# Optimization experiments

Measured on AMD Instinct MI355X. Metric: run time of the kernel, lower is better.

Reference implementation:

```python
import jax, jax.numpy as jnp
import numpy as np

HID, DSTATE, K, DIN, HDIM, NH, CHUNK = 2048, 128, 4, 4096, 64, 64, 256
CONVD = DIN + 2 * DSTATE  # 4352
EPS = 1e-5


def setup_inputs() -> dict:
    key = jax.random.key(0)
    ks = jax.random.split(key, 10)
    B, L = 2, 4096
    hidden_states = jax.random.normal(ks[0], (B, L, HID), jnp.float32)
    proj_out = 2 * (DIN + DSTATE) + NH  # 8512
    in_proj_w = jax.random.normal(ks[1], (proj_out, HID), jnp.float32) * (HID ** -0.5)
    conv_w = jax.random.normal(ks[2], (CONVD, K), jnp.float32) * (K ** -0.5)
    conv_b = jax.random.normal(ks[3], (CONVD,), jnp.float32) * 0.01
    dt_bias = jax.random.uniform(ks[4], (NH,), jnp.float32)
    A = jax.random.uniform(ks[5], (NH,), jnp.float32, minval=1.0, maxval=16.0)
    A_log = jnp.log(A)
    D = jnp.ones((NH,), jnp.float32)
    norm_w = jnp.ones((DIN,), jnp.float32)
    out_proj_w = jax.random.normal(ks[6], (HID, DIN), jnp.float32) * (DIN ** -0.5)
    return {"hidden_states": hidden_states, "in_proj_w": in_proj_w, "conv_w": conv_w,
            "conv_b": conv_b, "dt_bias": dt_bias, "A_log": A_log, "D": D,
            "norm_w": norm_w, "out_proj_w": out_proj_w}


def _segsum(x):
    # x: [..., L] -> [..., L, L] lower-triangular cumulative sums, -inf above diag
    Lc = x.shape[-1]
    cs = jnp.cumsum(x, -1)
    seg = cs[..., :, None] - cs[..., None, :]
    mask = jnp.tril(jnp.ones((Lc, Lc), bool))
    return jnp.where(mask, seg, -jnp.inf)


def _causal_conv1d(x, w, b):
    # x: [B, L, D] depthwise causal conv, kernel K, then SiLU
    L = x.shape[1]
    xp = jnp.pad(x, ((0, 0), (K - 1, 0), (0, 0)))
    y = sum(xp[:, i:i + L, :] * w[:, i] for i in range(K)) + b
    return jax.nn.silu(y)


def _ssd(x, Bm, Cm, dt, A, D):
    # x:[b,l,h,p]  Bm,Cm:[b,l,n]  dt:[b,l,h] (post-softplus)  A:[h]  D:[h]
    b, l, h, p = x.shape
    n = Bm.shape[-1]
    c = l // CHUNK
    xr = x.reshape(b, c, CHUNK, h, p)
    Br = Bm.reshape(b, c, CHUNK, n)
    Cr = Cm.reshape(b, c, CHUNK, n)
    dtr = dt.reshape(b, c, CHUNK, h)
    Adt = jnp.transpose(dtr * A, (0, 3, 1, 2))          # [b,h,c,L]
    Acs = jnp.cumsum(Adt, -1)                            # [b,h,c,L]
    Lmat = jnp.exp(_segsum(Adt))                         # [b,h,c,L,L]
    xdt = xr * dtr[..., None]                            # [b,c,L,h,p]
    # intra-chunk (diagonal) term
    Yd = jnp.einsum('bcln,bcsn,bhcls,bcshp->bclhp', Cr, Br, Lmat, xdt)
    # per-chunk final states
    decay_states = jnp.exp(Acs[..., -1:] - Acs)          # [b,h,c,L]
    chunk_states = jnp.einsum('bcln,bhcl,bclhp->bchpn', Br, decay_states, xdt)
    chunk_decay = jnp.exp(Acs[..., -1])                  # [b,h,c]
    def step(state, inp):
        dec, cs = inp
        return state * dec[..., None, None] + cs, state
    init = jnp.zeros((b, h, p, n), x.dtype)
    _, prev = jax.lax.scan(step, init,
                           (jnp.moveaxis(chunk_decay, -1, 0), jnp.moveaxis(chunk_states, 1, 0)))
    prev = jnp.moveaxis(prev, 0, 1)                      # [b,c,h,p,n] state entering each chunk
    Yo = jnp.einsum('bcln,bchpn,bhcl->bclhp', Cr, prev, jnp.exp(Acs))
    Y = Yd + Yo + xr * D[:, None]
    return Y.reshape(b, l, h * p)


def _gated_rmsnorm(y, z, w):
    y32 = y.astype(jnp.float32) * jax.nn.silu(z.astype(jnp.float32))
    var = jnp.mean(y32 * y32, -1, keepdims=True)
    return (y32 * jax.lax.rsqrt(var + EPS) * w).astype(y.dtype)


def reference(hidden_states, in_proj_w, conv_w, conv_b, dt_bias, A_log, D, norm_w, out_proj_w):
    zxbcdt = hidden_states @ in_proj_w.T                 # [b,l,8512]
    z = zxbcdt[..., :DIN]
    xBC = zxbcdt[..., DIN:DIN + CONVD]
    dt = zxbcdt[..., DIN + CONVD:]                       # [b,l,h]
    xBC = _causal_conv1d(xBC, conv_w, conv_b)
    x = xBC[..., :DIN]
    Bm = xBC[..., DIN:DIN + DSTATE]
    Cm = xBC[..., DIN + DSTATE:]
    A = -jnp.exp(A_log)
    dt = jax.nn.softplus(dt + dt_bias)
    b, l, _ = x.shape
    y = _ssd(x.reshape(b, l, NH, HDIM), Bm, Cm, dt, A, D)
    y = _gated_rmsnorm(y, z, norm_w)
    return y @ out_proj_w.T
```

## Files before the change

kernel.cpp:

```cpp
#include <hip/hip_runtime.h>
#include <hip/hip_bf16.h>


typedef __bf16 v8bf __attribute__((ext_vector_type(8)));
typedef float  v4f  __attribute__((ext_vector_type(4)));

#define LL long long

__device__ inline v8bf load8(const float* p) {
    v4f a = *(const v4f*)p, b = *(const v4f*)(p + 4);
    v8bf r;
#pragma unroll
    for (int i = 0; i < 4; ++i) { r[i] = (__bf16)a[i]; r[i + 4] = (__bf16)b[i]; }
    return r;
}

__device__ __forceinline__ void gload_lds16(const __bf16* g, __bf16* l) {
    __builtin_amdgcn_global_load_lds(
        (const __attribute__((address_space(1))) void*)g,
        (__attribute__((address_space(3))) void*)l, 16, 0, 0);
}

__global__ __launch_bounds__(256) void cast_bf16_kernel(
    const float* __restrict__ in, __bf16* __restrict__ out)
{
    LL i = ((LL)blockIdx.x * 256 + threadIdx.x) * 8;
    *(v8bf*)&out[i] = load8(&in[i]);
}

__global__ __launch_bounds__(256) void cast_split_kernel(
    const float* __restrict__ in, __bf16* __restrict__ hi,
    __bf16* __restrict__ lo)
{
    LL i = ((LL)blockIdx.x * 256 + threadIdx.x) * 8;
    v4f a = *(const v4f*)&in[i], b = *(const v4f*)&in[i + 4];
    v8bf h, l;
#pragma unroll
    for (int k = 0; k < 4; ++k) {
        __bf16 hh = (__bf16)a[k];  h[k]     = hh;  l[k]     = (__bf16)(a[k] - (float)hh);
        __bf16 hb = (__bf16)b[k];  h[k + 4] = hb;  l[k + 4] = (__bf16)(b[k] - (float)hb);
    }
    *(v8bf*)&hi[i] = h;
    *(v8bf*)&lo[i] = l;
}

template <int MODE, int TM, int TN, int RN>
__global__ __launch_bounds__(512, 2) void gemm_bt_8p(
    const __bf16* __restrict__ Ab, const __bf16* __restrict__ Bb, int KT,
    int lda, int ldb,
    __bf16* __restrict__ z_out, __bf16* __restrict__ x_out,
    float* __restrict__ outf, int ldc)
{
    __shared__ __align__(16) __bf16 lds[65536];
    constexpr int RM = 8 / RN;
    constexpr int LM = TM / RM, LN = TN / RN;
    const int orig = blockIdx.x;
    const int x = orig & 7, loc = orig >> 3;
    const int M0 = ((x / RN) * LM + loc / LN) * 256;
    const int N0 = ((x % RN) * LN + loc % LN) * 256;

    const int tid  = threadIdx.x;
    const int lane = tid & 63, wave = tid >> 6;
    const int wr = wave >> 2, wc = wave & 3;
    const int lrow = lane & 15, quad = lane >> 4;
    const int row0 = tid >> 3;
    const int g0   = (tid & 7) ^ (row0 & 7);

    v4f acc[8][4] = {};
    v8bf aF[2][4], b0F[2][2], b1F[2][2];

#define STAGE_A(par, half, kt) do { \
    const __bf16* _s = Ab + (size_t)(M0 + (half)*128 + row0) * lda + (kt)*64 + g0*8; \
    __bf16* _d = lds + ((par)*2 + (half)) * 8192 + wave * 512; \
    gload_lds16(_s, _d); \
    gload_lds16(_s + (size_t)64 * lda, _d + 4096); \
} while (0)

#define STAGE_B(par, half, kt) do { \
    const __bf16* _s = Bb + (size_t)(N0 + (half)*128 + row0) * ldb + (kt)*64 + g0*8; \
    __bf16* _d = lds + 32768 + ((par)*2 + (half)) * 8192 + wave * 512; \
    gload_lds16(_s, _d); \
    gload_lds16(_s + (size_t)64 * ldb, _d + 4096); \
} while (0)

#define READ_A(par, qm) do { \
    const __bf16* _s = lds + ((par)*2 + wr) * 8192; \
    _Pragma("unroll") \
    for (int _ks = 0; _ks < 2; ++_ks) \
      _Pragma("unroll") \
      for (int _m = 0; _m < 4; ++_m) \
        aF[_ks][_m] = *(const v8bf*)&_s[((qm)*64 + _m*16 + lrow)*64 + \
                                        ((((_ks<<2)+quad) ^ (lrow&7))<<3)]; \
} while (0)

#define READ_B(par, qn, DST) do { \
    const __bf16* _s = lds + 32768 + ((par)*2 + (wc>>1)) * 8192; \
    _Pragma("unroll") \
    for (int _ks = 0; _ks < 2; ++_ks) \
      _Pragma("unroll") \
      for (int _n = 0; _n < 2; ++_n) \
        DST[_ks][_n] = *(const v8bf*)&_s[((wc&1)*64 + (qn)*32 + _n*16 + lrow)*64 + \
                                         ((((_ks<<2)+quad) ^ (lrow&7))<<3)]; \
} while (0)

#define MFQ(qm, qn, BF) do { \
    __builtin_amdgcn_s_setprio(1); \
    _Pragma("unroll") \
    for (int _ks = 0; _ks < 2; ++_ks) \
      _Pragma("unroll") \
      for (int _m = 0; _m < 4; ++_m) \
        _Pragma("unroll") \
        for (int _n = 0; _n < 2; ++_n) \
          acc[(qm)*4+_m][(qn)*2+_n] = __builtin_amdgcn_mfma_f32_16x16x32_bf16( \
              aF[_ks][_m], BF[_ks][_n], acc[(qm)*4+_m][(qn)*2+_n], 0, 0, 0); \
    __builtin_amdgcn_s_setprio(0); \
} while (0)

#define PBAR  __builtin_amdgcn_s_barrier()
#define LGKM0 asm volatile("s_waitcnt lgkmcnt(0)" ::: "memory")
#define VMC4  asm volatile("s_waitcnt vmcnt(4)" ::: "memory")
#define VMC0  asm volatile("s_waitcnt vmcnt(0)" ::: "memory")

    STAGE_A(0, 0, 0); STAGE_A(0, 1, 0); STAGE_B(0, 0, 0); STAGE_B(0, 1, 0);
    STAGE_A(1, 0, 1); STAGE_B(1, 0, 1);
    VMC4; PBAR;

    const int KT2 = KT >> 1;
    for (int it = 0; it < KT2; ++it) {
        const int T0 = 2 * it, T1 = 2 * it + 1;
        const bool notlast = (it < KT2 - 1);
        READ_A(0, 0); READ_B(0, 0, b0F);
        STAGE_A(1, 1, T1);
        PBAR; LGKM0; MFQ(0, 0, b0F); PBAR;
        READ_B(0, 1, b1F);
        STAGE_B(1, 1, T1);
        PBAR; LGKM0; MFQ(0, 1, b1F); PBAR;
        READ_A(0, 1);
        if (notlast) STAGE_B(0, 0, T0 + 2);
        PBAR; LGKM0; MFQ(1, 0, b0F); PBAR;
        if (notlast) STAGE_A(0, 0, T0 + 2);
        PBAR; LGKM0; MFQ(1, 1, b1F);
        if (notlast) { VMC4; } else { VMC0; }
        PBAR;
        READ_A(1, 0); READ_B(1, 0, b0F);
        if (notlast) STAGE_A(0, 1, T0 + 2);
        PBAR; LGKM0; MFQ(0, 0, b0F); PBAR;
        READ_B(1, 1, b1F);
        if (notlast) STAGE_B(0, 1, T0 + 2);
        PBAR; LGKM0; MFQ(0, 1, b1F); PBAR;
        READ_A(1, 1);
        if (notlast) STAGE_B(1, 0, T1 + 2);
        PBAR; LGKM0; MFQ(1, 0, b0F); PBAR;
        if (notlast) STAGE_A(1, 0, T1 + 2);
        PBAR; LGKM0; MFQ(1, 1, b1F);
        if (notlast) { VMC4; } else { VMC0; }
        PBAR;
    }

#undef STAGE_A
#undef STAGE_B
#undef READ_A
#undef READ_B
#undef MFQ

#pragma unroll
    for (int m = 0; m < 8; ++m)
#pragma unroll
        for (int n = 0; n < 4; ++n)
#pragma unroll
            for (int r = 0; r < 4; ++r) {
                int row = M0 + wr * 128 + m * 16 + quad * 4 + r;
                int col = N0 + wc * 64 + n * 16 + lrow;
                float v = acc[m][n][r];
                if constexpr (MODE == 1) {
                    if (col < 4096) z_out[(LL)row * 4096 + col] = (__bf16)v;
                    else            x_out[(LL)row * 4096 + (col - 4096)] = (__bf16)v;
                } else {
                    outf[(LL)row * ldc + col] = v;
                }
            }
}

__global__ __launch_bounds__(256) void bcdt_gemm_kernel(
    const __bf16* __restrict__ Ahi, const __bf16* __restrict__ Alo,
    const __bf16* __restrict__ Whi, const __bf16* __restrict__ Wlo,
    const float* __restrict__ dtbi,
    float* __restrict__ bcr, float* __restrict__ dt)
{
    __shared__ __align__(16) __bf16 sAh[128 * 64];
    __shared__ __align__(16) __bf16 sAl[128 * 64];
    __shared__ __align__(16) __bf16 sWh[64 * 64];
    __shared__ __align__(16) __bf16 sWl[64 * 64];
    const int orig = blockIdx.x;
    const int swz = (orig & 7) * 40 + (orig >> 3);
    const int m0 = (swz / 5) * 128;
    const int n0 = (swz % 5) * 64;
    const int tid = threadIdx.x;
    const int lane = tid & 63, wave = tid >> 6;
    const int lrow = lane & 15, quad = lane >> 4;
    const int wm = wave * 32;
    v4f acc[2][4] = {};

    for (int k0 = 0; k0 < 2048; k0 += 64) {
#pragma unroll
        for (int i = 0; i < 4; ++i) {
            int e = tid + i * 256;
            int row = e >> 3, g = (e & 7) ^ (row & 7);
            const LL so = (LL)(m0 + row) * 2048 + k0 + g * 8;
            gload_lds16(&Ahi[so], &sAh[wave * 512 + i * 2048]);
            gload_lds16(&Alo[so], &sAl[wave * 512 + i * 2048]);
        }
#pragma unroll
        for (int i = 0; i < 2; ++i) {
            int e = tid + i * 256;
            int row = e >> 3, g = (e & 7) ^ (row & 7);
            const LL so = (LL)(n0 + row) * 2048 + k0 + g * 8;
            gload_lds16(&Whi[so], &sWh[wave * 512 + i * 2048]);
            gload_lds16(&Wlo[so], &sWl[wave * 512 + i * 2048]);
        }
        __syncthreads();
#pragma unroll
        for (int ks = 0; ks < 2; ++ks) {
            v8bf ah[2], al[2], wh[4], wl[4];
#pragma unroll
            for (int i = 0; i < 2; ++i) {
                int r = wm + i * 16 + lrow;
                int c = ((((ks << 2) + quad) ^ (lrow & 7)) << 3);
                ah[i] = *(const v8bf*)&sAh[r * 64 + c];
                al[i] = *(const v8bf*)&sAl[r * 64 + c];
            }
#pragma unroll
            for (int j = 0; j < 4; ++j) {
                int r = j * 16 + lrow;
                int c = ((((ks << 2) + quad) ^ (lrow & 7)) << 3);
                wh[j] = *(const v8bf*)&sWh[r * 64 + c];
                wl[j] = *(const v8bf*)&sWl[r * 64 + c];
            }
#pragma unroll
            for (int i = 0; i < 2; ++i)
#pragma unroll
                for (int j = 0; j < 4; ++j) {
                    acc[i][j] = __builtin_amdgcn_mfma_f32_16x16x32_bf16(ah[i], wh[j], acc[i][j], 0, 0, 0);
                    acc[i][j] = __builtin_amdgcn_mfma_f32_16x16x32_bf16(ah[i], wl[j], acc[i][j], 0, 0, 0);
                    acc[i][j] = __builtin_amdgcn_mfma_f32_16x16x32_bf16(al[i], wh[j], acc[i][j], 0, 0, 0);
                }
        }
        __syncthreads();
    }
#pragma unroll
    for (int i = 0; i < 2; ++i)
#pragma unroll
        for (int j = 0; j < 4; ++j)
#pragma unroll
            for (int r = 0; r < 4; ++r) {
                int row = m0 + wm + i * 16 + quad * 4 + r;
                int sc = n0 + j * 16 + lrow;
                float v = acc[i][j][r];
                if (sc < 256) {
                    bcr[(LL)row * 256 + sc] = v;
                } else {
                    float x = v + dtbi[sc - 256];
                    dt[row * 64 + (sc - 256)] = (x > 20.f) ? x : log1pf(__expf(x));
                }
            }
}

__global__ __launch_bounds__(256) void conv_x_kernel(
    const __bf16* __restrict__ xp, const float* __restrict__ cw,
    const float* __restrict__ cbias, __bf16* __restrict__ xq)
{
    int ch = blockIdx.x * 256 + threadIdx.x;
    int l = blockIdx.y, b = blockIdx.z;
    float acc = cbias[ch];
#pragma unroll
    for (int i = 0; i < 4; ++i) {
        int ls = l - 3 + i;
        if (ls >= 0)
            acc += (float)xp[((LL)b * 4096 + ls) * 4096 + ch] * cw[ch * 4 + i];
    }
    acc = acc / (1.f + __expf(-acc));
    xq[((LL)b * 4096 + l) * 4096 + ch] = (__bf16)acc;
}

__global__ __launch_bounds__(256) void conv_bc_kernel(
    const float* __restrict__ bcr, const float* __restrict__ cw,
    const float* __restrict__ cbias, float* __restrict__ bcc)
{
    int ch = threadIdx.x;
    int l = blockIdx.y, b = blockIdx.z;
    float acc = cbias[4096 + ch];
#pragma unroll
    for (int i = 0; i < 4; ++i) {
        int ls = l - 3 + i;
        if (ls >= 0)
            acc += bcr[((LL)b * 4096 + ls) * 256 + ch] * cw[(4096 + ch) * 4 + i];
    }
    acc = acc / (1.f + __expf(-acc));
    bcc[((LL)b * 4096 + l) * 256 + ch] = acc;
}

__global__ __launch_bounds__(256) void cumsum_kernel(
    const float* __restrict__ dt, const float* __restrict__ alog,
    float* __restrict__ acs, float* __restrict__ cdec)
{
    int h = blockIdx.x, c = blockIdx.y, b = blockIdx.z;
    int s = threadIdx.x;
    __shared__ float buf[256];
    float Av = -expf(alog[h]);
    int bl = b * 4096 + c * 256 + s;
    buf[s] = dt[bl * 64 + h] * Av;
    __syncthreads();
    for (int off = 1; off < 256; off <<= 1) {
        float v = (s >= off) ? buf[s - off] : 0.f;
        __syncthreads();
        buf[s] += v;
        __syncthreads();
    }
    int abase = (((b * 16) + c) * 64 + h) * 256;
    acs[abase + s] = buf[s];
    if (s == 255) cdec[(b * 64 + h) * 16 + c] = expf(buf[s]);
}

__global__ __launch_bounds__(256) void chunk_state_kernel(
    const __bf16* __restrict__ xq, const float* __restrict__ bcc,
    const float* __restrict__ dtb, const float* __restrict__ acs,
    float* __restrict__ cs)
{
    int h = blockIdx.x, c = blockIdx.y, b = blockIdx.z;
    int t = threadIdx.x;
    int lg = t & 63, pg = t >> 6;
    int n0 = lg * 2;
    __shared__ __align__(16) float xdt_s[64 * 68];
    __shared__ float dec_s[64];
    const LL lbase = (LL)b * 4096 + c * 256;
    const int abase = (((b * 16) + c) * 64 + h) * 256;
    float alast = acs[abase + 255];
    float a0[16] = {}, a1[16] = {};
    for (int st = 0; st < 4; ++st) {
        for (int i = 0; i < 16; ++i) {
            int e = t + i * 256; int sp = e >> 6, p = e & 63;
            LL row = lbase + st * 64 + sp;
            xdt_s[sp * 68 + p] = (float)xq[row * 4096 + h * 64 + p] * dtb[(row << 6) + h];
        }
        if (t < 64) dec_s[t] = __expf(alast - acs[abase + st * 64 + t]);
        __syncthreads();
        for (int sp = 0; sp < 64; ++sp) {
            LL row = lbase + st * 64 + sp;
            float2 bb = *(const float2*)&bcc[row * 256 + n0];
            float dd = dec_s[sp];
            float b0 = bb.x * dd, b1 = bb.y * dd;
#pragma unroll
            for (int q = 0; q < 4; ++q) {
                v4f xv = *(const v4f*)&xdt_s[sp * 68 + pg * 16 + q * 4];
#pragma unroll
                for (int j = 0; j < 4; ++j) { a0[q * 4 + j] += b0 * xv[j]; a1[q * 4 + j] += b1 * xv[j]; }
            }
        }
        __syncthreads();
    }
    const LL obase = ((LL)(((b * 16) + c) * 64 + h)) * 8192;
    for (int pp = 0; pp < 16; ++pp) {
        int p = pg * 16 + pp;
        cs[obase + p * 128 + n0]     = a0[pp];
        cs[obase + p * 128 + n0 + 1] = a1[pp];
    }
}

__global__ __launch_bounds__(256) void scan_kernel(
    float* __restrict__ cs, const float* __restrict__ cdec)
{
    int h = blockIdx.x, b = blockIdx.y;
    int t = threadIdx.x;
    float st[32];
#pragma unroll
    for (int i = 0; i < 32; ++i) st[i] = 0.f;
    for (int c = 0; c < 16; ++c) {
        LL base = ((LL)(((b * 16) + c) * 64 + h)) * 8192;
        float cd = cdec[(b * 64 + h) * 16 + c];
#pragma unroll
        for (int i = 0; i < 32; ++i) {
            int e = i * 256 + t;
            float v = cs[base + e];
            cs[base + e] = st[i];
            st[i] = st[i] * cd + v;
        }
    }
}

__global__ __launch_bounds__(256) void cb_kernel(const float* __restrict__ bcc,
                                                 float* __restrict__ cbt)
{
    int bx = blockIdx.x;
    int st = bx & 3, lh = bx >> 2;
    int c = blockIdx.y, b = blockIdx.z;
    int t = threadIdx.x;
    int lg = t & 63, pg = t >> 6;
    __shared__ float cr_s[128 * 33];
    __shared__ __align__(16) float brT[32 * 68];
    const LL lbase = (LL)b * 4096 + c * 256;
    const int l0 = lh * 128;
    float acc[2][16] = {};
    for (int nt = 0; nt < 4; ++nt) {
        for (int i = 0; i < 16; ++i) {
            int e = t + i * 256; int l = e >> 5, np = e & 31;
            cr_s[l * 33 + np] = bcc[(lbase + l0 + l) * 256 + 128 + nt * 32 + np];
        }
        for (int i = 0; i < 8; ++i) {
            int e = t + i * 256; int sp = e >> 5, np = e & 31;
            brT[np * 68 + sp] = bcc[(lbase + st * 64 + sp) * 256 + nt * 32 + np];
        }
        __syncthreads();
        for (int np = 0; np < 32; ++np) {
            float w0 = cr_s[lg * 33 + np], w1 = cr_s[(lg + 64) * 33 + np];
#pragma unroll
            for (int q = 0; q < 4; ++q) {
                v4f bv = *(const v4f*)&brT[np * 68 + pg * 16 + q * 4];
#pragma unroll
                for (int j = 0; j < 4; ++j) {
                    acc[0][q * 4 + j] += w0 * bv[j];
                    acc[1][q * 4 + j] += w1 * bv[j];
                }
            }
        }
        __syncthreads();
    }
    const LL obase = ((LL)((b * 16) + c)) * 65536;
#pragma unroll
    for (int r = 0; r < 2; ++r)
        for (int sp = 0; sp < 16; ++sp) {
            int s = st * 64 + pg * 16 + sp;
            cbt[obase + (LL)s * 256 + (l0 + lg + r * 64)] = acc[r][sp];
        }
}

__global__ __launch_bounds__(256) void ssd_y_kernel(
    __bf16* __restrict__ xq, const float* __restrict__ bcc,
    const float* __restrict__ dtb, const float* __restrict__ acs,
    const float* __restrict__ cbt, const float* __restrict__ prevS,
    const float* __restrict__ Dv)
{
    const int h = blockIdx.x, c = blockIdx.y, b = blockIdx.z;
    const int t = threadIdx.x;
    const int lane = t & 63, wave = t >> 6;
    const int lrow = lane & 15, quad = lane >> 4;
    const int wm = wave * 64;
    __shared__ __align__(16) __bf16 As[256][72];
    __shared__ __align__(16) __bf16 Bs[64 * 64];
    __shared__ float acs_s[256];
    __shared__ float qbuf[4][64];
    const LL lbase = (LL)b * 4096 + c * 256;
    const int abase = (((b * 16) + c) * 64 + h) * 256;
    acs_s[t] = acs[abase + t];
    __syncthreads();
    qbuf[t >> 6][t & 63] = __expf(acs_s[(t >> 6) * 64 + 63] - acs_s[t]);
    const float acl_t = acs_s[t];
    const float ea_t  = __expf(acl_t);
    __syncthreads();
    const LL cbbase = ((LL)((b * 16) + c)) * 65536;
    const LL pbase  = ((LL)(((b * 16) + c) * 64 + h)) * 8192;
    v4f acc[4][4] = {};

    for (int kb = 0; kb < 6; ++kb) {
        if (kb < 4) {
            const int sb = kb * 64;
            if (kb < wave) {
                const float r = __expf(acl_t - acs_s[sb + 63]);
#pragma unroll
                for (int g = 0; g < 8; ++g) {
                    v8bf wv;
#pragma unroll
                    for (int u = 0; u < 8; ++u) {
                        float cbv = cbt[cbbase + (LL)(sb + g * 8 + u) * 256 + t];
                        wv[u] = (__bf16)(cbv * (r * qbuf[kb][g * 8 + u]));
                    }
                    *(v8bf*)&As[t][g * 8] = wv;
                }
            } else if (kb == wave) {
#pragma unroll
                for (int g = 0; g < 8; ++g) {
                    v8bf wv;
#pragma unroll
                    for (int u = 0; u < 8; ++u) {
                        int s = sb + g * 8 + u;
                        float cbv = cbt[cbbase + (LL)s * 256 + t];
                        float d = acl_t - acs_s[s];
                        wv[u] = (__bf16)((s <= t) ? cbv * __expf(d) : 0.f);
                    }
                    *(v8bf*)&As[t][g * 8] = wv;
                }
            }
#pragma unroll
            for (int i = 0; i < 16; ++i) {
                int e = t + i * 256; int p = e & 63, sp = e >> 6;
                LL row = lbase + sb + sp;
                float xv = (float)xq[row * 4096 + h * 64 + p] * dtb[((int)row) * 64 + h];
                Bs[p * 64 + ((((sp >> 3) ^ (p & 7)) << 3) | (sp & 7))] = (__bf16)xv;
            }
        } else {
            const int nb = (kb - 4) * 64;
            const LL cb0 = (lbase + t) * 256 + 128 + nb;
#pragma unroll
            for (int g = 0; g < 8; ++g) {
                v4f c0 = *(const v4f*)&bcc[cb0 + g * 8];
                v4f c1 = *(const v4f*)&bcc[cb0 + g * 8 + 4];
                v8bf wv;
#pragma unroll
                for (int u = 0; u < 4; ++u) {
                    wv[u]     = (__bf16)(c0[u] * ea_t);
                    wv[u + 4] = (__bf16)(c1[u] * ea_t);
                }
                *(v8bf*)&As[t][g * 8] = wv;
            }
#pragma unroll
            for (int i = 0; i < 16; ++i) {
                int e = t + i * 256; int n = e & 63, p = e >> 6;
                float pv = prevS[pbase + (LL)p * 128 + nb + n];
                Bs[p * 64 + ((((n >> 3) ^ (p & 7)) << 3) | (n & 7))] = (__bf16)pv;
            }
        }
        __syncthreads();
        if (kb >= 4 || wave >= kb) {
#pragma unroll
            for (int ks = 0; ks < 2; ++ks) {
                v8bf af[4], bfv[4];
#pragma unroll
                for (int i = 0; i < 4; ++i)
                    af[i] = *(const v8bf*)&As[wm + i * 16 + lrow][ks * 32 + quad * 8];
#pragma unroll
                for (int j = 0; j < 4; ++j) {
                    int p = j * 16 + lrow;
                    int kg = (ks * 4 + quad) ^ (p & 7);
                    bfv[j] = *(const v8bf*)&Bs[p * 64 + kg * 8];
                }
#pragma unroll
                for (int i = 0; i < 4; ++i)
#pragma unroll
                    for (int j = 0; j < 4; ++j)
                        acc[i][j] = __builtin_amdgcn_mfma_f32_16x16x32_bf16(af[i], bfv[j], acc[i][j], 0, 0, 0);
            }
        }
        __syncthreads();
    }
    const float Dh = Dv[h];
#pragma unroll
    for (int i = 0; i < 4; ++i)
#pragma unroll
        for (int j = 0; j < 4; ++j)
#pragma unroll
            for (int r = 0; r < 4; ++r) {
                int l = wm + i * 16 + quad * 4 + r;
                int p = j * 16 + lrow;
                LL idx = (lbase + l) * 4096 + h * 64 + p;
                float v = acc[i][j][r] + Dh * (float)xq[idx];
                xq[idx] = (__bf16)v;
            }
}

__global__ __launch_bounds__(256) void rmsnorm_kernel(
    __bf16* __restrict__ y, const __bf16* __restrict__ z,
    const float* __restrict__ nw)
{
    LL r = blockIdx.x;
    int t = threadIdx.x;
    float vals[16]; float ss = 0.f;
#pragma unroll
    for (int i = 0; i < 16; ++i) {
        int j = i * 256 + t;
        float yv = (float)y[r * 4096 + j];
        float zv = (float)z[r * 4096 + j];
        float v = yv * (zv / (1.f + __expf(-zv)));
        vals[i] = v; ss += v * v;
    }
#pragma unroll
    for (int off = 32; off >= 1; off >>= 1) ss += __shfl_down(ss, off, 64);
    __shared__ float red[4];
    if ((t & 63) == 0) red[t >> 6] = ss;
    __syncthreads();
    float tot = red[0] + red[1] + red[2] + red[3];
    float rstd = rsqrtf(tot * (1.f / 4096.f) + 1e-5f);
#pragma unroll
    for (int i = 0; i < 16; ++i) {
        int j = i * 256 + t;
        y[r * 4096 + j] = (__bf16)(vals[i] * rstd * nw[j]);
    }
}

extern "C" void kernel_launch(void* const* d_in, const int* in_sizes, int n_in,
                              void* d_out, int out_size, void* d_ws, size_t ws_size,
                              hipStream_t stream) {
    const float* hs    = (const float*)d_in[0];
    const float* w1    = (const float*)d_in[1];
    const float* cw    = (const float*)d_in[2];
    const float* cbias = (const float*)d_in[3];
    const float* dtbi  = (const float*)d_in[4];
    const float* alog  = (const float*)d_in[5];
    const float* Dv    = (const float*)d_in[6];
    const float* nw    = (const float*)d_in[7];
    const float* wo    = (const float*)d_in[8];
    float* out = (float*)d_out;
    (void)in_sizes; (void)n_in; (void)out_size; (void)ws_size;

    char* ws = (char*)d_ws;
    size_t off = 0;
    auto alloc = [&](size_t bytes) { void* p = ws + off; off += (bytes + 255) & ~(size_t)255; return p; };
    __bf16* xp_b  = (__bf16*)alloc((size_t)8192 * 4096 * 2);
    __bf16* xq_b  = (__bf16*)alloc((size_t)8192 * 4096 * 2);
    float*  bcr_f = (float*) alloc((size_t)8192 * 256 * 4);
    float*  bcc_f = (float*) alloc((size_t)8192 * 256 * 4);
    float*  dt_f  = (float*) alloc((size_t)8192 * 64 * 4);
    float*  acs_f = (float*) alloc((size_t)2 * 16 * 64 * 256 * 4);
    float*  cd_f  = (float*) alloc((size_t)2 * 64 * 16 * 4);
    float*  cbt_f = (float*) alloc((size_t)2 * 16 * 256 * 256 * 4);
    float*  cs_f  = (float*)xp_b;
    __bf16* z_b   = (__bf16*)d_out;

    __bf16* hs_b  = xq_b;
    __bf16* w1_b  = xq_b + (size_t)8192 * 2048;
    __bf16* hs_lo = (__bf16*)xp_b;
    __bf16* ws_hi = hs_lo + (size_t)8192 * 2048;
    __bf16* ws_lo = ws_hi + (size_t)320 * 2048;
    __bf16* wo_b  = (__bf16*)xp_b;

    cast_split_kernel<<<8192, 256, 0, stream>>>(hs, hs_b, hs_lo);
    cast_bf16_kernel<<<8192, 256, 0, stream>>>(w1, w1_b);
    cast_split_kernel<<<320, 256, 0, stream>>>(w1 + (size_t)8192 * 2048, ws_hi, ws_lo);
    bcdt_gemm_kernel<<<320, 256, 0, stream>>>(hs_b, hs_lo, ws_hi, ws_lo,
                                              dtbi, bcr_f, dt_f);
    gemm_bt_8p<1, 32, 32, 4><<<dim3(1024), 512, 0, stream>>>(
        hs_b, w1_b, 32, 2048, 2048, z_b, xp_b, nullptr, 0);
    conv_x_kernel<<<dim3(16, 4096, 2), 256, 0, stream>>>(xp_b, cw, cbias, xq_b);
    conv_bc_kernel<<<dim3(1, 4096, 2), 256, 0, stream>>>(bcr_f, cw, cbias, bcc_f);
    cumsum_kernel<<<dim3(64, 16, 2), 256, 0, stream>>>(dt_f, alog, acs_f, cd_f);
    chunk_state_kernel<<<dim3(64, 16, 2), 256, 0, stream>>>(xq_b, bcc_f, dt_f, acs_f, cs_f);
    scan_kernel<<<dim3(64, 2), 256, 0, stream>>>(cs_f, cd_f);
    cb_kernel<<<dim3(8, 16, 2), 256, 0, stream>>>(bcc_f, cbt_f);
    ssd_y_kernel<<<dim3(64, 16, 2), 256, 0, stream>>>(xq_b, bcc_f, dt_f, acs_f, cbt_f, cs_f, Dv);
    cast_bf16_kernel<<<4096, 256, 0, stream>>>(wo, wo_b);
    rmsnorm_kernel<<<8192, 256, 0, stream>>>(xq_b, z_b, nw);
    gemm_bt_8p<2, 32, 8, 1><<<dim3(256), 512, 0, stream>>>(
        xq_b, wo_b, 64, 4096, 4096, nullptr, nullptr, out, 2048);
}
```

Before: 1.458 ms.

## Split SSD output kernel by row halves and skip upper-triangular CB tiles

The CB kernel now stores its output row-major (l-major) with vectorized float4 writes and launches only the 6 lower-triangular tiles. The SSD output kernel is split into two 128-thread blocks per chunk, each handling half the rows, so it skips the causally masked key blocks. It reads CB rows with vector loads and XOR-swizzles the A tile in shared memory. This removes wasted triangular work and strided global reads, in exchange for twice as many blocks and redundant loads of the B tile across the halves.

Measured after the change: 1.180 ms. 19.0% less time.

```diff
diff --git a/kernel.cpp b/kernel.cpp
--- a/kernel.cpp
+++ b/kernel.cpp
@@ -391,7 +391,8 @@
                                                  float* __restrict__ cbt)
 {
     int bx = blockIdx.x;
-    int st = bx & 3, lh = bx >> 2;
+    int lh = (bx < 2) ? 0 : 1;
+    int st = (bx < 2) ? bx : bx - 2;
     int c = blockIdx.y, b = blockIdx.z;
     int t = threadIdx.x;
     int lg = t & 63, pg = t >> 6;
@@ -399,7 +400,7 @@
     __shared__ __align__(16) float brT[32 * 68];
     const LL lbase = (LL)b * 4096 + c * 256;
     const int l0 = lh * 128;
-    float acc[2][16] = {};
+    v4f acc[2][4] = {};
     for (int nt = 0; nt < 4; ++nt) {
         for (int i = 0; i < 16; ++i) {
             int e = t + i * 256; int l = e >> 5, np = e & 31;
@@ -415,90 +416,106 @@
 #pragma unroll
             for (int q = 0; q < 4; ++q) {
                 v4f bv = *(const v4f*)&brT[np * 68 + pg * 16 + q * 4];
-#pragma unroll
-                for (int j = 0; j < 4; ++j) {
-                    acc[0][q * 4 + j] += w0 * bv[j];
-                    acc[1][q * 4 + j] += w1 * bv[j];
-                }
+                acc[0][q] += w0 * bv;
+                acc[1][q] += w1 * bv;
             }
         }
         __syncthreads();
     }
     const LL obase = ((LL)((b * 16) + c)) * 65536;
 #pragma unroll
-    for (int r = 0; r < 2; ++r)
-        for (int sp = 0; sp < 16; ++sp) {
-            int s = st * 64 + pg * 16 + sp;
-            cbt[obase + (LL)s * 256 + (l0 + lg + r * 64)] = acc[r][sp];
-        }
-}
-
-__global__ __launch_bounds__(256) void ssd_y_kernel(
+    for (int r = 0; r < 2; ++r) {
+        LL rowb = obase + (LL)(l0 + lg + r * 64) * 256 + st * 64 + pg * 16;
+#pragma unroll
+        for (int q = 0; q < 4; ++q)
+            *(v4f*)&cbt[rowb + q * 4] = acc[r][q];
+    }
+}
+
+__global__ __launch_bounds__(128) void ssd_y_kernel(
     __bf16* __restrict__ xq, const float* __restrict__ bcc,
     const float* __restrict__ dtb, const float* __restrict__ acs,
-    const float* __restrict__ cbt, const float* __restrict__ prevS,
+    const float* __restrict__ cbtT, const float* __restrict__ prevS,
     const float* __restrict__ Dv)
 {
-    const int h = blockIdx.x, c = blockIdx.y, b = blockIdx.z;
+    const int h = blockIdx.x;
+    const int c = blockIdx.y >> 1, lh = blockIdx.y & 1;
+    const int b = blockIdx.z;
     const int t = threadIdx.x;
     const int lane = t & 63, wave = t >> 6;
     const int lrow = lane & 15, quad = lane >> 4;
-    const int wm = wave * 64;
-    __shared__ __align__(16) __bf16 As[256][72];
+    const int rb = lh * 2 + wave;
+    const int l = lh * 128 + t;
+    __shared__ __align__(16) __bf16 As[128 * 64];
     __shared__ __align__(16) __bf16 Bs[64 * 64];
     __shared__ float acs_s[256];
     __shared__ float qbuf[4][64];
     const LL lbase = (LL)b * 4096 + c * 256;
     const int abase = (((b * 16) + c) * 64 + h) * 256;
     acs_s[t] = acs[abase + t];
+    acs_s[t + 128] = acs[abase + t + 128];
     __syncthreads();
-    qbuf[t >> 6][t & 63] = __expf(acs_s[(t >> 6) * 64 + 63] - acs_s[t]);
-    const float acl_t = acs_s[t];
+    qbuf[t >> 6][t & 63]       = __expf(acs_s[(t >> 6) * 64 + 63] - acs_s[t]);
+    qbuf[2 + (t >> 6)][t & 63] = __expf(acs_s[(2 + (t >> 6)) * 64 + 63] - acs_s[128 + t]);
+    const float acl_t = acs_s[l];
     const float ea_t  = __expf(acl_t);
     __syncthreads();
     const LL cbbase = ((LL)((b * 16) + c)) * 65536;
     const LL pbase  = ((LL)(((b * 16) + c) * 64 + h)) * 8192;
+    const int rbmax = lh * 2 + 1;
     v4f acc[4][4] = {};
 
     for (int kb = 0; kb < 6; ++kb) {
+        if (kb < 4 && kb > rbmax) continue;
         if (kb < 4) {
             const int sb = kb * 64;
-            if (kb < wave) {
-                const float r = __expf(acl_t - acs_s[sb + 63]);
-#pragma unroll
-                for (int g = 0; g < 8; ++g) {
-                    v8bf wv;
-#pragma unroll
-                    for (int u = 0; u < 8; ++u) {
-                        float cbv = cbt[cbbase + (LL)(sb + g * 8 + u) * 256 + t];
-                        wv[u] = (__bf16)(cbv * (r * qbuf[kb][g * 8 + u]));
+            if (kb <= rb) {
+                const LL crow = cbbase + (LL)l * 256 + sb;
+                if (kb < rb) {
+                    const float rf = __expf(acl_t - acs_s[sb + 63]);
+#pragma unroll
+                    for (int g = 0; g < 8; ++g) {
+                        v4f c0 = *(const v4f*)&cbtT[crow + g * 8];
+                        v4f c1 = *(const v4f*)&cbtT[crow + g * 8 + 4];
+                        v8bf wv;
+#pragma unroll
+                        for (int u = 0; u < 4; ++u) {
+                            wv[u]     = (__bf16)(c0[u] * (rf * qbuf[kb][g * 8 + u]));
+                            wv[u + 4] = (__bf16)(c1[u] * (rf * qbuf[kb][g * 8 + 4 + u]));
+                        }
+                        *(v8bf*)&As[t * 64 + ((g ^ (t & 7)) << 3)] = wv;
                     }
-                    *(v8bf*)&As[t][g * 8] = wv;
+                } else {
+#pragma unroll
+                    for (int g = 0; g < 8; ++g) {
+                        v4f c0 = *(const v4f*)&cbtT[crow + g * 8];
+                        v4f c1 = *(const v4f*)&cbtT[crow + g * 8 + 4];
+                        v8bf wv;
+#pragma unroll
+                        for (int u = 0; u < 4; ++u) {
+                            int s0 = sb + g * 8 + u, s1 = s0 + 4;
+                            wv[u]     = (__bf16)((s0 <= l) ? c0[u] * __expf(acl_t - acs_s[s0]) : 0.f);
+                            wv[u + 4] = (__bf16)((s1 <= l) ? c1[u] * __expf(acl_t - acs_s[s1]) : 0.f);
+                        }
+                        *(v8bf*)&As[t * 64 + ((g ^ (t & 7)) << 3)] = wv;
+                    }
                 }
-            } else if (kb == wave) {
-#pragma unroll
-                for (int g = 0; g < 8; ++g) {
-                    v8bf wv;
-#pragma unroll
-                    for (int u = 0; u < 8; ++u) {
-                        int s = sb + g * 8 + u;
-                        float cbv = cbt[cbbase + (LL)s * 256 + t];
-                        float d = acl_t - acs_s[s];
-                        wv[u] = (__bf16)((s <= t) ? cbv * __expf(d) : 0.f);
-                    }
-                    *(v8bf*)&As[t][g * 8] = wv;
-                }
             }
 #pragma unroll
             for (int i = 0; i < 16; ++i) {
-                int e = t + i * 256; int p = e & 63, sp = e >> 6;
+                int e = t + i * 128; int pp = e & 31, sp = e >> 5;
+                int p = pp * 2;
                 LL row = lbase + sb + sp;
-                float xv = (float)xq[row * 4096 + h * 64 + p] * dtb[((int)row) * 64 + h];
-                Bs[p * 64 + ((((sp >> 3) ^ (p & 7)) << 3) | (sp & 7))] = (__bf16)xv;
+                float dv = dtb[((int)row) * 64 + h];
+                ushort2 xu = *(const ushort2*)&xq[row * 4096 + h * 64 + p];
+                __bf16 x0, x1;
+                *(unsigned short*)&x0 = xu.x; *(unsigned short*)&x1 = xu.y;
+                Bs[p * 64 + ((((sp >> 3) ^ (p & 7)) << 3) | (sp & 7))] = (__bf16)((float)x0 * dv);
+                Bs[(p + 1) * 64 + ((((sp >> 3) ^ ((p + 1) & 7)) << 3) | (sp & 7))] = (__bf16)((float)x1 * dv);
             }
         } else {
             const int nb = (kb - 4) * 64;
-            const LL cb0 = (lbase + t) * 256 + 128 + nb;
+            const LL cb0 = (lbase + l) * 256 + 128 + nb;
 #pragma unroll
             for (int g = 0; g < 8; ++g) {
                 v4f c0 = *(const v4f*)&bcc[cb0 + g * 8];
@@ -509,23 +526,29 @@
                     wv[u]     = (__bf16)(c0[u] * ea_t);
                     wv[u + 4] = (__bf16)(c1[u] * ea_t);
                 }
-                *(v8bf*)&As[t][g * 8] = wv;
+                *(v8bf*)&As[t * 64 + ((g ^ (t & 7)) << 3)] = wv;
             }
 #pragma unroll
             for (int i = 0; i < 16; ++i) {
-                int e = t + i * 256; int n = e & 63, p = e >> 6;
-                float pv = prevS[pbase + (LL)p * 128 + nb + n];
-                Bs[p * 64 + ((((n >> 3) ^ (p & 7)) << 3) | (n & 7))] = (__bf16)pv;
-            }
-        }
-        __syncthreads();
-        if (kb >= 4 || wave >= kb) {
+                int e = t + i * 128; int nn = e & 31, p = e >> 5;
+                int n = nn * 2;
+                float2 pv = *(const float2*)&prevS[pbase + (LL)p * 128 + nb + n];
+                int chunk = ((n >> 3) ^ (p & 7));
+                __bf16 b0 = (__bf16)pv.x, b1 = (__bf16)pv.y;
+                __bf16* dst = &Bs[p * 64 + (chunk << 3) + (n & 7)];
+                dst[0] = b0; dst[1] = b1;
+            }
+        }
+        __syncthreads();
+        if (kb >= 4 || kb <= rb) {
 #pragma unroll
             for (int ks = 0; ks < 2; ++ks) {
                 v8bf af[4], bfv[4];
 #pragma unroll
-                for (int i = 0; i < 4; ++i)
-                    af[i] = *(const v8bf*)&As[wm + i * 16 + lrow][ks * 32 + quad * 8];
+                for (int i = 0; i < 4; ++i) {
+                    int row = wave * 64 + i * 16 + lrow;
+                    af[i] = *(const v8bf*)&As[row * 64 + ((((ks << 2) + quad) ^ (lrow & 7)) << 3)];
+                }
 #pragma unroll
                 for (int j = 0; j < 4; ++j) {
                     int p = j * 16 + lrow;
@@ -548,9 +571,9 @@
         for (int j = 0; j < 4; ++j)
 #pragma unroll
             for (int r = 0; r < 4; ++r) {
-                int l = wm + i * 16 + quad * 4 + r;
+                int ll = lh * 128 + wave * 64 + i * 16 + quad * 4 + r;
                 int p = j * 16 + lrow;
-                LL idx = (lbase + l) * 4096 + h * 64 + p;
+                LL idx = (lbase + ll) * 4096 + h * 64 + p;
                 float v = acc[i][j][r] + Dh * (float)xq[idx];
                 xq[idx] = (__bf16)v;
             }
@@ -633,8 +656,8 @@
     cumsum_kernel<<<dim3(64, 16, 2), 256, 0, stream>>>(dt_f, alog, acs_f, cd_f);
     chunk_state_kernel<<<dim3(64, 16, 2), 256, 0, stream>>>(xq_b, bcc_f, dt_f, acs_f, cs_f);
     scan_kernel<<<dim3(64, 2), 256, 0, stream>>>(cs_f, cd_f);
-    cb_kernel<<<dim3(8, 16, 2), 256, 0, stream>>>(bcc_f, cbt_f);
-    ssd_y_kernel<<<dim3(64, 16, 2), 256, 0, stream>>>(xq_b, bcc_f, dt_f, acs_f, cbt_f, cs_f, Dv);
+    cb_kernel<<<dim3(6, 16, 2), 256, 0, stream>>>(bcc_f, cbt_f);
+    ssd_y_kernel<<<dim3(64, 32, 2), 128, 0, stream>>>(xq_b, bcc_f, dt_f, acs_f, cbt_f, cs_f, Dv);
     cast_bf16_kernel<<<4096, 256, 0, stream>>>(wo, wo_b);
     rmsnorm_kernel<<<8192, 256, 0, stream>>>(xq_b, z_b, nw);
     gemm_bt_8p<2, 32, 8, 1><<<dim3(256), 512, 0, stream>>>(
```
